# Kernel tuning notes

Measured on AMD Instinct MI355X. Metric: run time of the kernel, lower is better.

Reference implementation:

```python
import jax, jax.numpy as jnp
import numpy as np

B, S, HID, NH, HD = 2, 2048, 1024, 16, 64
SCALE = 1.0 / np.sqrt(HD)
NEG = -1e9


def _rope_cache(seq_len, dim, base=10000.0):
    inv_freq = 1.0 / (base ** (np.arange(0, dim, 2, dtype=np.float32) / dim))
    t = np.arange(seq_len, dtype=np.float32)
    freqs = np.outer(t, inv_freq)                      # [S, dim/2]
    emb = np.concatenate([freqs, freqs], axis=-1)      # [S, dim]
    return jnp.asarray(np.cos(emb)), jnp.asarray(np.sin(emb))


def _rotate_half(x):
    x1, x2 = jnp.split(x, 2, axis=-1)
    return jnp.concatenate([-x2, x1], axis=-1)


def setup_inputs() -> dict:
    key = jax.random.key(0)
    k0, k1, k2, k3, k4 = jax.random.split(key, 5)
    hidden_states = jax.random.normal(k0, (B, S, HID), jnp.float32)
    Wq = jax.random.normal(k1, (HID, NH * HD), jnp.float32) * 0.02
    Wk = jax.random.normal(k2, (HID, NH * HD), jnp.float32) * 0.02
    Wv = jax.random.normal(k3, (HID, NH * HD), jnp.float32) * 0.02
    Wo = jax.random.normal(k4, (NH * HD, HID), jnp.float32) * 0.02
    causal = jnp.tril(jnp.ones((S, S), bool))
    attention_mask = jnp.broadcast_to(
        jnp.where(causal, 0.0, NEG).astype(jnp.float32)[None, None], (B, 1, S, S))
    position_ids = jnp.broadcast_to(jnp.arange(S, dtype=jnp.int32)[None], (B, S))
    cos, sin = _rope_cache(S, HD)
    return {"hidden_states": hidden_states, "attention_mask": attention_mask,
            "position_ids": position_ids, "cos": cos, "sin": sin,
            "Wq": Wq, "Wk": Wk, "Wv": Wv, "Wo": Wo}


def reference(hidden_states, attention_mask, position_ids, cos, sin, Wq, Wk, Wv, Wo):
    b, s, _ = hidden_states.shape
    def proj(W):  # [B,S,HID] @ [HID,NH*HD] -> [B,NH,S,HD]
        return jnp.einsum('bsh,hd->bsd', hidden_states, W).reshape(b, s, NH, HD).transpose(0, 2, 1, 3)
    q, k, v = proj(Wq), proj(Wk), proj(Wv)
    # RoPE: gather per-position cos/sin -> [B,1,S,HD]
    cos_g = cos[position_ids][:, None]
    sin_g = sin[position_ids][:, None]
    q = q * cos_g + _rotate_half(q) * sin_g
    k = k * cos_g + _rotate_half(k) * sin_g
    scores = jnp.einsum('bhqd,bhkd->bhqk', q, k) * SCALE + attention_mask
    attn = jax.nn.softmax(scores.astype(jnp.float32), axis=-1).astype(q.dtype)
    out = jnp.einsum('bhqk,bhkd->bhqd', attn, v)
    out = out.transpose(0, 2, 1, 3).reshape(b, s, NH * HD)
    return jnp.einsum('bsd,dh->bsh', out, Wo)
```

## Files before the change

kernel.cpp:

```cpp
#include <hip/hip_runtime.h>

typedef __bf16 bf16x8 __attribute__((ext_vector_type(8)));
typedef float  f32x4  __attribute__((ext_vector_type(4)));
typedef unsigned short ushortx8 __attribute__((ext_vector_type(8)));
typedef unsigned short ushortx4 __attribute__((ext_vector_type(4)));

static __device__ __forceinline__ unsigned short f2bf(float f) {
  unsigned int u = __builtin_bit_cast(unsigned int, f);
  u += 0x7FFFu + ((u >> 16) & 1u);
  return (unsigned short)(u >> 16);
}
static __device__ __forceinline__ unsigned short f2bf_fast(float f) {
  unsigned int u = __builtin_bit_cast(unsigned int, f);
  return (unsigned short)((u + 0x8000u) >> 16);
}

#define GLL16(gp, lp) __builtin_amdgcn_global_load_lds(                       \
    (const __attribute__((address_space(1))) void*)(gp),                      \
    (__attribute__((address_space(3))) void*)(lp), 16, 0, 0)

__global__ __launch_bounds__(256) void prep_kernel(const float* __restrict__ X,
                                                   const float* __restrict__ W0,
                                                   const float* __restrict__ W1,
                                                   const float* __restrict__ W2,
                                                   const float* __restrict__ W3,
                                                   unsigned short* __restrict__ Xbf,
                                                   unsigned short* __restrict__ D0,
                                                   unsigned short* __restrict__ D1,
                                                   unsigned short* __restrict__ D2,
                                                   unsigned short* __restrict__ D3) {
  int z = blockIdx.z;
  if (z >= 4) {
    long bid = (long)(z - 4) * 1024 + blockIdx.y * 32 + blockIdx.x;
    int tl = threadIdx.y * 32 + threadIdx.x;
    long i = bid * 2048 + (long)tl * 8;
    float4 f0 = *(const float4*)(X + i);
    float4 f1 = *(const float4*)(X + i + 4);
    ushortx8 u;
    u[0] = f2bf(f0.x); u[1] = f2bf(f0.y); u[2] = f2bf(f0.z); u[3] = f2bf(f0.w);
    u[4] = f2bf(f1.x); u[5] = f2bf(f1.y); u[6] = f2bf(f1.z); u[7] = f2bf(f1.w);
    *(ushortx8*)(Xbf + i) = u;
    return;
  }
  const float* src = (z == 0) ? W0 : (z == 1) ? W1 : (z == 2) ? W2 : W3;
  unsigned short* dst = (z == 0) ? D0 : (z == 1) ? D1 : (z == 2) ? D2 : D3;
  const int R = 1024, C = 1024;
  __shared__ unsigned short t[32][33];
  int c = blockIdx.x * 32 + threadIdx.x;
#pragma unroll
  for (int i = 0; i < 4; ++i) {
    int r = blockIdx.y * 32 + threadIdx.y + i * 8;
    t[threadIdx.y + i * 8][threadIdx.x] = f2bf(src[(size_t)r * C + c]);
  }
  __syncthreads();
  int rr = blockIdx.y * 32 + threadIdx.x;
#pragma unroll
  for (int i = 0; i < 4; ++i) {
    int cc = blockIdx.x * 32 + threadIdx.y + i * 8;
    dst[(size_t)cc * R + rr] = t[threadIdx.x][threadIdx.y + i * 8];
  }
}

__global__ __launch_bounds__(512, 2) void gemm256_kernel(
    const unsigned short* __restrict__ A,
    const unsigned short* __restrict__ BT0,
    const unsigned short* __restrict__ BT1,
    const unsigned short* __restrict__ BT2,
    unsigned short* __restrict__ outQ,
    unsigned short* __restrict__ outK,
    unsigned short* __restrict__ outVT,
    const int* __restrict__ pos_ids,
    const float* __restrict__ cosb,
    const float* __restrict__ sinb) {
  const int K = 1024;
  int id = blockIdx.x * 24 + blockIdx.y;
  int z = id >> 6;
  int r_ = id & 63;
  int n_idx = r_ & 3, m_idx = r_ >> 2;
  const unsigned short* BT = (z == 0) ? BT0 : (z == 1 ? BT1 : BT2);
  int m0 = m_idx * 256, n0 = n_idx * 256;
  int t = threadIdx.x, lane = t & 63, w = t >> 6;
  int wy = w >> 2, wx = w & 3;
  int n16 = lane & 15, quad = lane >> 4;

  __shared__ __align__(16) unsigned short sA[2][2][256][32];
  __shared__ __align__(16) unsigned short sB[2][2][256][32];

  const char* gA0 = (const char*)(A + (size_t)(m0 + (w & 3) * 16 + (lane >> 2)) * K
                                  + (w >> 2) * 32 + ((lane & 3) ^ ((lane >> 2) & 3)) * 8);
  const char* gB0 = (const char*)(BT + (size_t)(n0 + (w & 3) * 16 + (lane >> 2)) * K
                                  + (w >> 2) * 32 + ((lane & 3) ^ ((lane >> 2) & 3)) * 8);
  unsigned short* ldsA_w = &sA[0][w >> 2][(w & 3) * 16][0];
  unsigned short* ldsB_w = &sB[0][w >> 2][(w & 3) * 16][0];

  const unsigned short* rdA = &sA[0][0][wy * 128 + n16][(quad ^ (n16 & 3)) * 8];
  const unsigned short* rdB = &sB[0][0][wx * 64 + n16][(quad ^ (n16 & 3)) * 8];

  f32x4 acc[8][4];
#pragma unroll
  for (int i = 0; i < 8; ++i)
#pragma unroll
    for (int j = 0; j < 4; ++j) acc[i][j] = f32x4{0.f, 0.f, 0.f, 0.f};

  bf16x8 a[4][2], b[2][2];

#define STG_A(db, kt, H)                                                              \
  do {                                                                                \
    GLL16(gA0 + (size_t)((H) * 128) * 2048 + (kt) * 128,                              \
          ldsA_w + (db) * 16384 + ((H) * 128) * 32);                                  \
    GLL16(gA0 + (size_t)((H) * 128 + 64) * 2048 + (kt) * 128,                         \
          ldsA_w + (db) * 16384 + ((H) * 128 + 64) * 32);                             \
  } while (0)
#define STG_B(db, kt, H)                                                              \
  do {                                                                                \
    GLL16(gB0 + (size_t)((H) * 128) * 2048 + (kt) * 128,                              \
          ldsB_w + (db) * 16384 + ((H) * 128) * 32);                                  \
    GLL16(gB0 + (size_t)((H) * 128 + 64) * 2048 + (kt) * 128,                         \
          ldsB_w + (db) * 16384 + ((H) * 128 + 64) * 32);                             \
  } while (0)

#define RD_A(db, mh)                                                                  \
  do {                                                                                \
    _Pragma("unroll") for (int i = 0; i < 4; ++i) {                                   \
      a[i][0] = *(const bf16x8*)(rdA + (db) * 16384 + ((mh) * 64 + i * 16) * 32);     \
      a[i][1] = *(const bf16x8*)(rdA + (db) * 16384 + 8192 + ((mh) * 64 + i * 16) * 32); \
    }                                                                                 \
  } while (0)
#define RD_B(db, nh)                                                                  \
  do {                                                                                \
    _Pragma("unroll") for (int jj = 0; jj < 2; ++jj) {                                \
      b[jj][0] = *(const bf16x8*)(rdB + (db) * 16384 + ((nh) * 32 + jj * 16) * 32);   \
      b[jj][1] = *(const bf16x8*)(rdB + (db) * 16384 + 8192 + ((nh) * 32 + jj * 16) * 32); \
    }                                                                                 \
  } while (0)

#define MM(mh, nh)                                                                    \
  do {                                                                                \
    _Pragma("unroll") for (int i = 0; i < 4; ++i)                                     \
      _Pragma("unroll") for (int jj = 0; jj < 2; ++jj) {                              \
        acc[(mh) * 4 + i][(nh) * 2 + jj] = __builtin_amdgcn_mfma_f32_16x16x32_bf16(   \
            a[i][0], b[jj][0], acc[(mh) * 4 + i][(nh) * 2 + jj], 0, 0, 0);            \
        acc[(mh) * 4 + i][(nh) * 2 + jj] = __builtin_amdgcn_mfma_f32_16x16x32_bf16(   \
            a[i][1], b[jj][1], acc[(mh) * 4 + i][(nh) * 2 + jj], 0, 0, 0);            \
      }                                                                               \
  } while (0)

#define BARRIER_MFMA(mh, nh, VM)                                                      \
  do {                                                                                \
    if (VM) asm volatile("s_waitcnt vmcnt(0)" ::: "memory");                          \
    __builtin_amdgcn_s_barrier();                                                     \
    asm volatile("s_waitcnt lgkmcnt(0)" ::: "memory");                                \
    __builtin_amdgcn_sched_barrier(0);                                                \
    __builtin_amdgcn_s_setprio(1);                                                    \
    MM(mh, nh);                                                                       \
    __builtin_amdgcn_s_setprio(0);                                                    \
    __builtin_amdgcn_sched_barrier(0);                                                \
    __builtin_amdgcn_s_barrier();                                                     \
  } while (0)

  STG_A(0, 0, 0); STG_A(0, 0, 1); STG_B(0, 0, 0); STG_B(0, 0, 1);
  asm volatile("s_waitcnt vmcnt(0)" ::: "memory");
  __builtin_amdgcn_s_barrier();

  for (int j = 0; j < 8; ++j) {
    int t1 = 2 * j + 1, t2 = 2 * j + 2;
    bool more = (j < 7);
    RD_A(0, 0); RD_B(0, 0);
    STG_A(1, t1, 0); STG_A(1, t1, 1);
    BARRIER_MFMA(0, 0, 0);
    RD_B(0, 1);
    STG_B(1, t1, 0); STG_B(1, t1, 1);
    BARRIER_MFMA(0, 1, 0);
    RD_A(0, 1);
    BARRIER_MFMA(1, 1, 0);
    RD_B(0, 0);
    BARRIER_MFMA(1, 0, 1);
    RD_A(1, 0); RD_B(1, 0);
    if (more) { STG_A(0, t2, 0); STG_A(0, t2, 1); }
    BARRIER_MFMA(0, 0, 0);
    RD_B(1, 1);
    if (more) { STG_B(0, t2, 0); STG_B(0, t2, 1); }
    BARRIER_MFMA(0, 1, 0);
    RD_A(1, 1);
    BARRIER_MFMA(1, 1, 0);
    RD_B(1, 0);
    BARRIER_MFMA(1, 0, 1);
  }
#undef STG_A
#undef STG_B
#undef RD_A
#undef RD_B
#undef MM
#undef BARRIER_MFMA

  if (z < 2) {
    const float qs = (z == 0) ? (0.125f * 1.44269504088896340736f) : 1.0f;
#pragma unroll
    for (int mi = 0; mi < 8; ++mi)
#pragma unroll
      for (int r = 0; r < 4; ++r) {
        int row = m0 + wy * 128 + mi * 16 + quad * 4 + r;
        int b_ = row >> 11, s_ = row & 2047;
        int pos = pos_ids[b_ * 2048 + s_];
        const float* cb = cosb + (size_t)pos * 64;
        const float* sb = sinb + (size_t)pos * 64;
#pragma unroll
        for (int ni = 0; ni < 2; ++ni) {
          int d0 = ni * 16 + n16;
          float c0 = cb[d0] * qs, s0 = sb[d0] * qs;
          float c1 = cb[d0 + 32] * qs, s1 = sb[d0 + 32] * qs;
          float x0 = acc[mi][ni][r], x1 = acc[mi][ni + 2][r];
          acc[mi][ni][r]     = x0 * c0 - x1 * s0;
          acc[mi][ni + 2][r] = x1 * c1 + x0 * s1;
        }
      }
    unsigned short* dst = (z == 0) ? outQ : outK;
#pragma unroll
    for (int mi = 0; mi < 8; ++mi)
#pragma unroll
      for (int ni = 0; ni < 4; ++ni)
#pragma unroll
        for (int r = 0; r < 4; ++r) {
          int row = m0 + wy * 128 + mi * 16 + quad * 4 + r;
          int col = n0 + wx * 64 + ni * 16 + n16;
          int b_ = row >> 11, s_ = row & 2047, h_ = col >> 6, d_ = col & 63;
          dst[(((size_t)b_ * 16 + h_) * 2048 + s_) * 64 + d_] = f2bf(acc[mi][ni][r]);
        }
    return;
  }

#pragma unroll
  for (int mi = 0; mi < 8; ++mi)
#pragma unroll
    for (int ni = 0; ni < 4; ++ni) {
      int row = m0 + wy * 128 + mi * 16 + quad * 4;
      int b_ = row >> 11, s_ = row & 2047;
      int col = n0 + wx * 64 + ni * 16 + n16;
      int h_ = col >> 6, d_ = col & 63;
      ushortx4 u;
#pragma unroll
      for (int r = 0; r < 4; ++r) u[r] = f2bf(acc[mi][ni][r]);
      *(ushortx4*)(&outVT[(((size_t)b_ * 16 + h_) * 64 + d_) * 2048 + s_]) = u;
    }
}

__global__ __launch_bounds__(256) void gemm64_kernel(const unsigned short* __restrict__ A,
                                                     const unsigned short* __restrict__ BT,
                                                     float* __restrict__ outF) {
  const int K = 1024, N = 1024;
  int m0 = blockIdx.x * 64, n0 = blockIdx.y * 64;
  int t = threadIdx.x, lane = t & 63, w = t >> 6;
  int wy = w >> 1, wx = w & 1;
  int n16 = lane & 15, quad = lane >> 4;
  __shared__ __align__(16) unsigned short sA0[64 * 32];
  __shared__ __align__(16) unsigned short sA1[64 * 32];
  __shared__ __align__(16) unsigned short sB0[64 * 32];
  __shared__ __align__(16) unsigned short sB1[64 * 32];

  int r4 = lane >> 2, c4 = lane & 3;
  const char* gA = (const char*)(A + (size_t)(m0 + w * 16 + r4) * K) + ((c4 ^ (r4 & 3)) * 16);
  const char* gB = (const char*)(BT + (size_t)(n0 + w * 16 + r4) * K) + ((c4 ^ (r4 & 3)) * 16);

  f32x4 acc[2][2];
#pragma unroll
  for (int i = 0; i < 2; ++i)
#pragma unroll
    for (int j = 0; j < 2; ++j) acc[i][j] = f32x4{0.f, 0.f, 0.f, 0.f};

#define WSTAGE(kk_, SA, SB)                                                     \
  do {                                                                          \
    GLL16(gA + (size_t)(kk_) * 2, SA + (w * 16) * 32);                          \
    GLL16(gB + (size_t)(kk_) * 2, SB + (w * 16) * 32);                          \
  } while (0)

#define WCOMPUTE(SA, SB)                                                        \
  do {                                                                          \
    int cs = (quad ^ (n16 & 3)) * 8;                                            \
    bf16x8 a0 = *(const bf16x8*)(&SA[(wy * 32 + n16) * 32 + cs]);               \
    bf16x8 a1 = *(const bf16x8*)(&SA[(wy * 32 + 16 + n16) * 32 + cs]);          \
    bf16x8 b0 = *(const bf16x8*)(&SB[(wx * 32 + n16) * 32 + cs]);               \
    bf16x8 b1 = *(const bf16x8*)(&SB[(wx * 32 + 16 + n16) * 32 + cs]);          \
    acc[0][0] = __builtin_amdgcn_mfma_f32_16x16x32_bf16(a0, b0, acc[0][0], 0, 0, 0); \
    acc[0][1] = __builtin_amdgcn_mfma_f32_16x16x32_bf16(a0, b1, acc[0][1], 0, 0, 0); \
    acc[1][0] = __builtin_amdgcn_mfma_f32_16x16x32_bf16(a1, b0, acc[1][0], 0, 0, 0); \
    acc[1][1] = __builtin_amdgcn_mfma_f32_16x16x32_bf16(a1, b1, acc[1][1], 0, 0, 0); \
  } while (0)

  WSTAGE(0, sA0, sB0);
  for (int kk = 0; kk < K;) {
    __syncthreads();
    if (kk + 32 < K) WSTAGE(kk + 32, sA1, sB1);
    WCOMPUTE(sA0, sB0);
    kk += 32;
    if (kk >= K) break;
    __syncthreads();
    if (kk + 32 < K) WSTAGE(kk + 32, sA0, sB0);
    WCOMPUTE(sA1, sB1);
    kk += 32;
  }
#undef WSTAGE
#undef WCOMPUTE

#pragma unroll
  for (int mt = 0; mt < 2; ++mt)
#pragma unroll
    for (int nt = 0; nt < 2; ++nt)
#pragma unroll
      for (int r = 0; r < 4; ++r) {
        int row = m0 + wy * 32 + mt * 16 + quad * 4 + r;
        int col = n0 + wx * 32 + nt * 16 + n16;
        outF[(size_t)row * N + col] = acc[mt][nt][r];
      }
}

__global__ __launch_bounds__(512) void attn_kernel(const unsigned short* __restrict__ Q,
                                                   const unsigned short* __restrict__ Kk,
                                                   const unsigned short* __restrict__ VT,
                                                   unsigned short* __restrict__ O) {
  int bh = blockIdx.x;
  int qt = (int)(gridDim.y - 1 - blockIdx.y);
  int t = threadIdx.x;
  int lane = t & 63;
  int w = t >> 6;
  int g = w >> 2;
  int w4 = w & 3;
  int n16 = lane & 15, quad = lane >> 4;
  int r8 = lane >> 3, c8 = lane & 7;
  const unsigned short* Qb = Q + (size_t)bh * 2048 * 64;
  const unsigned short* Kb = Kk + (size_t)bh * 2048 * 64;
  const unsigned short* Vb = VT + (size_t)bh * 64 * 2048;

  __shared__ __align__(16) unsigned short sKV[2 * 2 * 2 * 4096];
  __shared__ __align__(16) unsigned short sP[8][16 * 64];
  unsigned short* spW = sP[w];
  unsigned short* gBase = sKV + g * 16384;

  int b_ = bh >> 4, h_ = bh & 15;
  int nk = qt + 1;
  int u = (nk + 1) >> 1;
  int beg = g ? u : 0;
  int end = g ? nk : u;
  int qg = qt * 64 + w4 * 16 + n16;

  bf16x8 aQ[2];
#pragma unroll
  for (int kb = 0; kb < 2; ++kb)
    aQ[kb] = *(const bf16x8*)(Qb + (size_t)qg * 64 + kb * 32 + quad * 8);

  f32x4 o[4];
  float mst = -3e38f, lst = 0.f;
#pragma unroll
  for (int ct = 0; ct < 4; ++ct) o[ct] = f32x4{0.f, 0.f, 0.f, 0.f};

#define ASTAGE(kt_, BUF)                                                                  \
  do {                                                                                    \
    const unsigned short* kg_ = Kb + (size_t)((kt_) * 64 + w4 * 16) * 64;                 \
    const unsigned short* vg_ = Vb + (size_t)(w4 * 16) * 2048 + (kt_) * 64;               \
    unsigned short* dK = gBase + (BUF) * 8192 + (w4 * 16) * 64;                           \
    unsigned short* dV = dK + 4096;                                                       \
    GLL16(kg_ + (size_t)r8 * 64 + (c8 ^ r8) * 8, dK);                                     \
    GLL16(kg_ + (size_t)(8 + r8) * 64 + (c8 ^ r8) * 8, dK + 8 * 64);                      \
    GLL16(vg_ + (size_t)r8 * 2048 + (c8 ^ r8) * 8, dV);                                   \
    GLL16(vg_ + (size_t)(8 + r8) * 2048 + (c8 ^ r8) * 8, dV + 8 * 64);                    \
  } while (0)

#define ACOMPUTE(kt_, BUF)                                                                \
  do {                                                                                    \
    const unsigned short* kT_ = gBase + (BUF) * 8192;                                     \
    const unsigned short* vT_ = kT_ + 4096;                                               \
    f32x4 sc[4];                                \
    _Pragma("unroll") for (int mt = 0; mt < 4; ++mt) {                                    \
      const unsigned short* kr = &kT_[(mt * 16 + n16) * 64];                              \
      bf16x8 ka0 = *(const bf16x8*)(kr + ((quad ^ (n16 & 7)) * 8));                       \
      bf16x8 ka1 = *(const bf16x8*)(kr + (((4 + quad) ^ (n16 & 7)) * 8));                 \
      f32x4 zv = f32x4{0.f, 0.f, 0.f, 0.f};                                               \
      zv = __builtin_amdgcn_mfma_f32_16x16x32_bf16(ka0, aQ[0], zv, 0, 0, 0);              \
      sc[mt] = __builtin_amdgcn_mfma_f32_16x16x32_bf16(ka1, aQ[1], zv, 0, 0, 0);          \
    }                                                                                     \
    float p[4][4];                                                                        \
    _Pragma("unroll") for (int mt = 0; mt < 4; ++mt)                                      \
      _Pragma("unroll") for (int r = 0; r < 4; ++r) p[mt][r] = sc[mt][r];                 \
    if ((kt_) == nk - 1) {                                 \
      int kb0 = (kt_) * 64 + quad * 4;                                                    \
      _Pragma("unroll") for (int mt = 0; mt < 4; ++mt)                                    \
        _Pragma("unroll") for (int r = 0; r < 4; ++r)                                     \
          if (kb0 + mt * 16 + r > qg) p[mt][r] = -3e38f;                                  \
    }                                                                                     \
    float rm = p[0][0];                                                                   \
    _Pragma("unroll") for (int mt = 0; mt < 4; ++mt)                                      \
      _Pragma("unroll") for (int r = 0; r < 4; ++r) rm = fmaxf(rm, p[mt][r]);             \
    rm = fmaxf(rm, __shfl_xor(rm, 16));                                                   \
    rm = fmaxf(rm, __shfl_xor(rm, 32));                                                   \
    float mn = fmaxf(mst, rm);                                                            \
    float al = exp2f(mst - mn);                                                           \
    mst = mn;                                                                             \
    float rs = 0.f;                                                                       \
    _Pragma("unroll") for (int mt = 0; mt < 4; ++mt)                                      \
      _Pragma("unroll") for (int r = 0; r < 4; ++r) {                                     \
        p[mt][r] = exp2f(p[mt][r] - mn);                                                  \
        rs += p[mt][r];                                                                   \
      }                                                                                   \
    lst = lst * al + rs;                                                                  \
    _Pragma("unroll") for (int ct = 0; ct < 4; ++ct)                                      \
      _Pragma("unroll") for (int r = 0; r < 4; ++r) o[ct][r] *= al;                       \
    _Pragma("unroll") for (int mt = 0; mt < 4; ++mt) {                                    \
      ushortx4 uu;                                                                        \
      _Pragma("unroll") for (int r = 0; r < 4; ++r) uu[r] = f2bf_fast(p[mt][r]);          \
      int ch = (mt * 2 + (quad >> 1)) ^ (n16 & 7);                                        \
      *(ushortx4*)(&spW[n16 * 64 + ch * 8 + (quad & 1) * 4]) = uu;                        \
    }                                                                                     \
    __builtin_amdgcn_s_waitcnt(0xC07F);     \
    bf16x8 aP0 = *(const bf16x8*)(&spW[n16 * 64 + ((quad ^ (n16 & 7)) * 8)]);             \
    bf16x8 aP1 = *(const bf16x8*)(&spW[n16 * 64 + (((4 + quad) ^ (n16 & 7)) * 8)]);       \
    _Pragma("unroll") for (int ct = 0; ct < 4; ++ct) {                                    \
      const unsigned short* vr = &vT_[(ct * 16 + n16) * 64];                              \
      bf16x8 va0 = *(const bf16x8*)(vr + ((quad ^ (n16 & 7)) * 8));                       \
      bf16x8 va1 = *(const bf16x8*)(vr + (((4 + quad) ^ (n16 & 7)) * 8));                 \
      o[ct] = __builtin_amdgcn_mfma_f32_16x16x32_bf16(va0, aP0, o[ct], 0, 0, 0);          \
      o[ct] = __builtin_amdgcn_mfma_f32_16x16x32_bf16(va1, aP1, o[ct], 0, 0, 0);          \
    }                                                                                     \
  } while (0)

  if (beg < end) ASTAGE(beg, 0);
  int it = 0;
  while (it < u) {
    __syncthreads();
    {
      int kt = beg + it;
      if (kt + 1 < end) ASTAGE(kt + 1, 1);
      if (kt < end) ACOMPUTE(kt, 0);
    }
    if (++it >= u) break;
    __syncthreads();
    {
      int kt = beg + it;
      if (kt + 1 < end) ASTAGE(kt + 1, 0);
      if (kt < end) ACOMPUTE(kt, 1);
    }
    ++it;
  }
#undef ASTAGE
#undef ACOMPUTE

  lst += __shfl_xor(lst, 16);
  lst += __shfl_xor(lst, 32);

  __syncthreads();
  float* scratch = (float*)sKV;
  int sidx = (w4 * 64 + lane) * 18;
  if (g == 1) {
#pragma unroll
    for (int ct = 0; ct < 4; ++ct)
#pragma unroll
      for (int r = 0; r < 4; ++r) scratch[sidx + ct * 4 + r] = o[ct][r];
    scratch[sidx + 16] = mst;
    scratch[sidx + 17] = lst;
  }
  __syncthreads();
  if (g == 0) {
    float m1 = scratch[sidx + 16], l1 = scratch[sidx + 17];
    float m = fmaxf(mst, m1);
    float a0 = exp2f(mst - m), a1 = exp2f(m1 - m);
    float inv = 1.0f / (lst * a0 + l1 * a1);
#pragma unroll
    for (int ct = 0; ct < 4; ++ct) {
      ushortx4 uo;
#pragma unroll
      for (int r = 0; r < 4; ++r) {
        float v = (o[ct][r] * a0 + scratch[sidx + ct * 4 + r] * a1) * inv;
        uo[r] = f2bf(v);
      }
      size_t addr = ((size_t)b_ * 2048 + qg) * 1024 + h_ * 64 + ct * 16 + quad * 4;
      *(ushortx4*)(&O[addr]) = uo;
    }
  }
}

extern "C" void kernel_launch(void* const* d_in, const int* in_sizes, int n_in,
                              void* d_out, int out_size, void* d_ws, size_t ws_size,
                              hipStream_t stream) {
  const float* X    = (const float*)d_in[0];
  const int*   pos  = (const int*)d_in[2];
  const float* cosb = (const float*)d_in[3];
  const float* sinb = (const float*)d_in[4];
  const float* Wq   = (const float*)d_in[5];
  const float* Wk   = (const float*)d_in[6];
  const float* Wv   = (const float*)d_in[7];
  const float* Wo   = (const float*)d_in[8];
  float* out = (float*)d_out;

  char* ws = (char*)d_ws;
  const size_t SZ_X = 4096UL * 1024 * 2;
  const size_t SZ_W = 1024UL * 1024 * 2;
  unsigned short* Xbf = (unsigned short*)(ws);
  unsigned short* WTq = (unsigned short*)(ws + SZ_X);
  unsigned short* WTk = (unsigned short*)(ws + SZ_X + SZ_W);
  unsigned short* WTv = (unsigned short*)(ws + SZ_X + 2 * SZ_W);
  unsigned short* WTo = (unsigned short*)(ws + SZ_X + 3 * SZ_W);
  unsigned short* Qbf = (unsigned short*)(ws + SZ_X + 4 * SZ_W);
  unsigned short* Kbf = (unsigned short*)(ws + 2 * SZ_X + 4 * SZ_W);
  unsigned short* VTr = (unsigned short*)(ws + 3 * SZ_X + 4 * SZ_W);
  unsigned short* Obf = (unsigned short*)(ws + 4 * SZ_X + 4 * SZ_W);

  prep_kernel<<<dim3(32, 32, 6), dim3(32, 8), 0, stream>>>(
      X, Wq, Wk, Wv, Wo, Xbf, WTq, WTk, WTv, WTo);

  gemm256_kernel<<<dim3(8, 24), 512, 0, stream>>>(Xbf, WTq, WTk, WTv,
                                                  Qbf, Kbf, VTr,
                                                  pos, cosb, sinb);

  attn_kernel<<<dim3(32, 32), 512, 0, stream>>>(Qbf, Kbf, VTr, Obf);

  gemm64_kernel<<<dim3(64, 16), 256, 0, stream>>>(Obf, WTo, out);
}
```

Before: 209.9 us.

## Restructure QKV GEMM mainloop into 4-stage LDS ring with 32-wide k tiles

New measurement: 206.0 us. Within noise of the previous version (-1.9%).

```diff
diff --git a/kernel.cpp b/kernel.cpp
--- a/kernel.cpp
+++ b/kernel.cpp
@@ -83,18 +83,20 @@
   int wy = w >> 2, wx = w & 3;
   int n16 = lane & 15, quad = lane >> 4;
 
-  __shared__ __align__(16) unsigned short sA[2][2][256][32];
-  __shared__ __align__(16) unsigned short sB[2][2][256][32];
-
-  const char* gA0 = (const char*)(A + (size_t)(m0 + (w & 3) * 16 + (lane >> 2)) * K
-                                  + (w >> 2) * 32 + ((lane & 3) ^ ((lane >> 2) & 3)) * 8);
-  const char* gB0 = (const char*)(BT + (size_t)(n0 + (w & 3) * 16 + (lane >> 2)) * K
-                                  + (w >> 2) * 32 + ((lane & 3) ^ ((lane >> 2) & 3)) * 8);
-  unsigned short* ldsA_w = &sA[0][w >> 2][(w & 3) * 16][0];
-  unsigned short* ldsB_w = &sB[0][w >> 2][(w & 3) * 16][0];
-
-  const unsigned short* rdA = &sA[0][0][wy * 128 + n16][(quad ^ (n16 & 3)) * 8];
-  const unsigned short* rdB = &sB[0][0][wx * 64 + n16][(quad ^ (n16 & 3)) * 8];
+  __shared__ __align__(16) unsigned short sA[4][256][32];
+  __shared__ __align__(16) unsigned short sB[4][256][32];
+  __shared__ __align__(16) unsigned short sDummy[512];
+
+  int schunk = (lane & 3) ^ ((lane >> 2) & 3) ^ ((lane >> 4) & 3);
+  const unsigned short* gA0 = A + (size_t)(m0 + w * 16 + (lane >> 2)) * K + schunk * 8;
+  const unsigned short* gB0 = BT + (size_t)(n0 + w * 16 + (lane >> 2)) * K + schunk * 8;
+  const size_t rstep = (size_t)128 * K;
+  unsigned short* stA = &sA[0][w * 16][0];
+  unsigned short* stB = &sB[0][w * 16][0];
+
+  int cs = (quad ^ (n16 & 3) ^ (n16 >> 2)) * 8;
+  const unsigned short* rdA = &sA[0][wy * 128 + n16][0] + cs;
+  const unsigned short* rdB = &sB[0][wx * 64 + n16][0] + cs;
 
   f32x4 acc[8][4];
 #pragma unroll
@@ -102,96 +104,78 @@
 #pragma unroll
     for (int j = 0; j < 4; ++j) acc[i][j] = f32x4{0.f, 0.f, 0.f, 0.f};
 
-  bf16x8 a[4][2], b[2][2];
-
-#define STG_A(db, kt, H)                                                              \
+  bf16x8 a[4], b[4];
+
+#define STG_A(tt, d0, d1)                                                             \
   do {                                                                                \
-    GLL16(gA0 + (size_t)((H) * 128) * 2048 + (kt) * 128,                              \
-          ldsA_w + (db) * 16384 + ((H) * 128) * 32);                                  \
-    GLL16(gA0 + (size_t)((H) * 128 + 64) * 2048 + (kt) * 128,                         \
-          ldsA_w + (db) * 16384 + ((H) * 128 + 64) * 32);                             \
-  } while (0)
-#define STG_B(db, kt, H)                                                              \
+    GLL16(gA0 + (size_t)(tt) * 32, (d0));                                             \
+    GLL16(gA0 + (size_t)(tt) * 32 + rstep, (d1));                                     \
+  } while (0)
+#define STG_B(tt, d0, d1)                                                             \
   do {                                                                                \
-    GLL16(gB0 + (size_t)((H) * 128) * 2048 + (kt) * 128,                              \
-          ldsB_w + (db) * 16384 + ((H) * 128) * 32);                                  \
-    GLL16(gB0 + (size_t)((H) * 128 + 64) * 2048 + (kt) * 128,                         \
-          ldsB_w + (db) * 16384 + ((H) * 128 + 64) * 32);                             \
-  } while (0)
-
-#define RD_A(db, mh)                                                                  \
-  do {                                                                                \
-    _Pragma("unroll") for (int i = 0; i < 4; ++i) {                                   \
-      a[i][0] = *(const bf16x8*)(rdA + (db) * 16384 + ((mh) * 64 + i * 16) * 32);     \
-      a[i][1] = *(const bf16x8*)(rdA + (db) * 16384 + 8192 + ((mh) * 64 + i * 16) * 32); \
-    }                                                                                 \
-  } while (0)
-#define RD_B(db, nh)                                                                  \
-  do {                                                                                \
-    _Pragma("unroll") for (int jj = 0; jj < 2; ++jj) {                                \
-      b[jj][0] = *(const bf16x8*)(rdB + (db) * 16384 + ((nh) * 32 + jj * 16) * 32);   \
-      b[jj][1] = *(const bf16x8*)(rdB + (db) * 16384 + 8192 + ((nh) * 32 + jj * 16) * 32); \
-    }                                                                                 \
-  } while (0)
-
-#define MM(mh, nh)                                                                    \
+    GLL16(gB0 + (size_t)(tt) * 32, (d0));                                             \
+    GLL16(gB0 + (size_t)(tt) * 32 + rstep, (d1));                                     \
+  } while (0)
+
+#define RD_A4(bufi, mh)                                                               \
   do {                                                                                \
     _Pragma("unroll") for (int i = 0; i < 4; ++i)                                     \
-      _Pragma("unroll") for (int jj = 0; jj < 2; ++jj) {                              \
+      a[i] = *(const bf16x8*)(rdA + (bufi) * 8192 + ((mh) * 64 + i * 16) * 32);       \
+  } while (0)
+#define RD_B4(bufi)                                                                   \
+  do {                                                                                \
+    _Pragma("unroll") for (int jb = 0; jb < 4; ++jb)                                  \
+      b[jb] = *(const bf16x8*)(rdB + (bufi) * 8192 + (jb) * 16 * 32);                 \
+  } while (0)
+
+#define MMQ(mh, nh)                                                                   \
+  do {                                                                                \
+    _Pragma("unroll") for (int i = 0; i < 4; ++i)                                     \
+      _Pragma("unroll") for (int jj = 0; jj < 2; ++jj)                                \
         acc[(mh) * 4 + i][(nh) * 2 + jj] = __builtin_amdgcn_mfma_f32_16x16x32_bf16(   \
-            a[i][0], b[jj][0], acc[(mh) * 4 + i][(nh) * 2 + jj], 0, 0, 0);            \
-        acc[(mh) * 4 + i][(nh) * 2 + jj] = __builtin_amdgcn_mfma_f32_16x16x32_bf16(   \
-            a[i][1], b[jj][1], acc[(mh) * 4 + i][(nh) * 2 + jj], 0, 0, 0);            \
-      }                                                                               \
-  } while (0)
-
-#define BARRIER_MFMA(mh, nh, VM)                                                      \
-  do {                                                                                \
-    if (VM) asm volatile("s_waitcnt vmcnt(0)" ::: "memory");                          \
-    __builtin_amdgcn_s_barrier();                                                     \
-    asm volatile("s_waitcnt lgkmcnt(0)" ::: "memory");                                \
-    __builtin_amdgcn_sched_barrier(0);                                                \
-    __builtin_amdgcn_s_setprio(1);                                                    \
-    MM(mh, nh);                                                                       \
-    __builtin_amdgcn_s_setprio(0);                                                    \
-    __builtin_amdgcn_sched_barrier(0);                                                \
-    __builtin_amdgcn_s_barrier();                                                     \
-  } while (0)
-
-  STG_A(0, 0, 0); STG_A(0, 0, 1); STG_B(0, 0, 0); STG_B(0, 0, 1);
-  asm volatile("s_waitcnt vmcnt(0)" ::: "memory");
+            a[i], b[(nh) * 2 + jj], acc[(mh) * 4 + i][(nh) * 2 + jj], 0, 0, 0);       \
+  } while (0)
+
+  STG_A(0, stA, stA + 4096);               STG_B(0, stB, stB + 4096);
+  STG_A(1, stA + 8192, stA + 12288);       STG_B(1, stB + 8192, stB + 12288);
+  STG_A(2, stA + 16384, stA + 20480);      STG_B(2, stB + 16384, stB + 20480);
+  asm volatile("s_waitcnt vmcnt(8)" ::: "memory");
   __builtin_amdgcn_s_barrier();
 
-  for (int j = 0; j < 8; ++j) {
-    int t1 = 2 * j + 1, t2 = 2 * j + 2;
-    bool more = (j < 7);
-    RD_A(0, 0); RD_B(0, 0);
-    STG_A(1, t1, 0); STG_A(1, t1, 1);
-    BARRIER_MFMA(0, 0, 0);
-    RD_B(0, 1);
-    STG_B(1, t1, 0); STG_B(1, t1, 1);
-    BARRIER_MFMA(0, 1, 0);
-    RD_A(0, 1);
-    BARRIER_MFMA(1, 1, 0);
-    RD_B(0, 0);
-    BARRIER_MFMA(1, 0, 1);
-    RD_A(1, 0); RD_B(1, 0);
-    if (more) { STG_A(0, t2, 0); STG_A(0, t2, 1); }
-    BARRIER_MFMA(0, 0, 0);
-    RD_B(1, 1);
-    if (more) { STG_B(0, t2, 0); STG_B(0, t2, 1); }
-    BARRIER_MFMA(0, 1, 0);
-    RD_A(1, 1);
-    BARRIER_MFMA(1, 1, 0);
-    RD_B(1, 0);
-    BARRIER_MFMA(1, 0, 1);
+#pragma unroll 4
+  for (int kt = 0; kt < 32; ++kt) {
+    int buf = kt & 3;
+    int pf = kt + 3;
+    bool ok = pf < 32;
+    int pfc = ok ? pf : 31;
+    unsigned short* dA0 = ok ? (stA + (pf & 3) * 8192) : sDummy;
+    unsigned short* dA1 = ok ? (dA0 + 4096) : sDummy;
+    unsigned short* dB0 = ok ? (stB + (pf & 3) * 8192) : sDummy;
+    unsigned short* dB1 = ok ? (dB0 + 4096) : sDummy;
+    RD_A4(buf, 0);
+    RD_B4(buf);
+    STG_A(pfc, dA0, dA1);
+    __builtin_amdgcn_s_barrier();
+    __builtin_amdgcn_s_setprio(1);
+    MMQ(0, 0); MMQ(0, 1);
+    __builtin_amdgcn_s_setprio(0);
+    __builtin_amdgcn_sched_barrier(0);
+    __builtin_amdgcn_s_barrier();
+    RD_A4(buf, 1);
+    STG_B(pfc, dB0, dB1);
+    __builtin_amdgcn_s_barrier();
+    __builtin_amdgcn_s_setprio(1);
+    MMQ(1, 0); MMQ(1, 1);
+    __builtin_amdgcn_s_setprio(0);
+    __builtin_amdgcn_sched_barrier(0);
+    asm volatile("s_waitcnt vmcnt(8)" ::: "memory");
+    __builtin_amdgcn_s_barrier();
   }
 #undef STG_A
 #undef STG_B
-#undef RD_A
-#undef RD_B
-#undef MM
-#undef BARRIER_MFMA
+#undef RD_A4
+#undef RD_B4
+#undef MMQ
 
   if (z < 2) {
     const float qs = (z == 0) ? (0.125f * 1.44269504088896340736f) : 1.0f;
```
